# Performance work log

Measured on AMD Instinct MI355X. Metric: run time of the kernel, lower is better.

## Reference

```python
import jax, jax.numpy as jnp
import numpy as np

V = 780        # junction-tree vocab size
N = 50000      # total nodes in batch
M = 100001     # total messages (+1 null slot at index 0)
K = 6          # padded max neighbors
H = 256        # hidden size
B = 64         # number of trees (scope entries)
DEPTH = 6      # GRU depth


def setup_inputs() -> dict:
    key = jax.random.key(0)
    ks = jax.random.split(key, 12)
    p = lambda k, s: jax.random.normal(k, s, jnp.float32) * 0.02
    return {
        "fnode": jax.random.randint(ks[0], (N,), 0, V),
        "fmess": jax.random.randint(ks[1], (M,), 0, N),
        "node_graph": jax.random.randint(ks[2], (N, K), 0, M),
        "mess_graph": jax.random.randint(ks[3], (M, K), 0, M),
        "scope_st": jax.random.randint(ks[4], (B,), 0, N),
        "emb": p(ks[5], (V, H)),
        "Wz": p(ks[6], (H, 2 * H)), "bz": jnp.zeros((H,), jnp.float32),
        "Wr": p(ks[7], (H, H)),
        "Ur": p(ks[8], (H, H)), "bu": jnp.zeros((H,), jnp.float32),
        "Wh": p(ks[9], (H, 2 * H)), "bh": jnp.zeros((H,), jnp.float32),
        "Wo": p(ks[10], (H, 2 * H)), "bo": jnp.zeros((H,), jnp.float32),
    }


def reference(fnode, fmess, node_graph, mess_graph, scope_st,
              emb, Wz, bz, Wr, Ur, bu, Wh, bh, Wo, bo):
    fnode_e = emb[fnode]                       # [N, H] embedded node features
    x = fnode_e[fmess]                         # [M, H] per-message source features
    mask = jnp.ones((M, 1), jnp.float32).at[0].set(0.0)  # zero the null message
    # W_r(x) depends only on x; hoist it out of the loop (same math as original)
    xWr = (x @ Wr.T)[:, None, :]               # [M, 1, H]

    h = jnp.zeros((M, H), jnp.float32)
    for _ in range(DEPTH):
        h_nei = h[mess_graph]                  # [M, K, H] gather neighbor messages
        sum_h = h_nei.sum(axis=1)              # [M, H]
        z = jax.nn.sigmoid(jnp.concatenate([x, sum_h], axis=1) @ Wz.T + bz)
        r = jax.nn.sigmoid(xWr + h_nei @ Ur.T + bu)   # [M, K, H]
        sum_gated_h = (r * h_nei).sum(axis=1)  # [M, H]
        pre_h = jnp.tanh(jnp.concatenate([x, sum_gated_h], axis=1) @ Wh.T + bh)
        h = ((1.0 - z) * sum_h + z * pre_h) * mask

    mess_nei = h[node_graph].sum(axis=1)       # [N, H]
    node_vecs = jax.nn.relu(
        jnp.concatenate([fnode_e, mess_nei], axis=-1) @ Wo.T + bo)  # [N, H]
    tree_vecs = node_vecs[scope_st]            # [B, H] root vector per tree
    return tree_vecs, h
```

## Files before the change

kernel.cpp:

```cpp
#include <hip/hip_runtime.h>

typedef unsigned short u16;
typedef unsigned int   u32;
typedef short bf16x8 __attribute__((ext_vector_type(8)));
typedef float f32x4  __attribute__((ext_vector_type(4)));

#define V_ 780
#define N_ 50000
#define M_ 100001
#define K_ 6
#define H_ 256
#define B_ 64
#define DEPTH_ 6

typedef __attribute__((address_space(3))) u32 lds_u32;
typedef __attribute__((address_space(1))) const u32 glb_u32;
__device__ __forceinline__ void dma16(const void* g, void* l){
  __builtin_amdgcn_global_load_lds((glb_u32*)g, (lds_u32*)l, 16, 0, 0);
}

__device__ __forceinline__ float b2f(u16 u){
  union { u32 i; float f; } x; x.i = ((u32)u) << 16; return x.f;
}
__device__ __forceinline__ u16 f2b(float f){
  union { float f; u32 i; } x; x.f = f;
  u32 r = x.i + 0x7fffu + ((x.i >> 16) & 1u);
  return (u16)(r >> 16);
}
__device__ __forceinline__ float rcp_(float x){ return __builtin_amdgcn_rcpf(x); }
__device__ __forceinline__ float sigm(float x){ return rcp_(1.f + __expf(-x)); }
__device__ __forceinline__ float tanh_(float x){
  x = fminf(fmaxf(x, -15.f), 15.f);
  float e = __expf(2.f*x);
  return (e - 1.f) * rcp_(e + 1.f);
}
__device__ __forceinline__ int swz(int r){ return (r + (r >> 2)) & 3; }

__global__ void k_tables(const float* __restrict__ emb,
    const float* __restrict__ Wz, const float* __restrict__ bz,
    const float* __restrict__ Wr, const float* __restrict__ bu,
    const float* __restrict__ Wh, const float* __restrict__ bh,
    const float* __restrict__ Wo, const float* __restrict__ bo,
    float* __restrict__ tWz, float* __restrict__ tXr,
    float* __restrict__ tWh, float* __restrict__ tWo){
  int v = blockIdx.x, q = blockIdx.y, j = threadIdx.x;
  __shared__ float e[H_];
  e[j] = emb[v*H_ + j];
  __syncthreads();
  const float* w; const float* b; float* o; int ld;
  if      (q == 0){ w = Wz; b = bz; o = tWz; ld = 2*H_; }
  else if (q == 1){ w = Wr; b = bu; o = tXr; ld = H_;   }
  else if (q == 2){ w = Wh; b = bh; o = tWh; ld = 2*H_; }
  else            { w = Wo; b = bo; o = tWo; ld = 2*H_; }
  const float* wr = w + (size_t)j*ld;
  float a0 = 0.f, a1 = 0.f;
  #pragma unroll 4
  for (int i = 0; i < H_; i += 8){
    float4 x = *(const float4*)(wr + i);
    float4 y = *(const float4*)(wr + i + 4);
    a0 += e[i  ]*x.x + e[i+1]*x.y + e[i+2]*x.z + e[i+3]*x.w;
    a1 += e[i+4]*y.x + e[i+5]*y.y + e[i+6]*y.z + e[i+7]*y.w;
  }
  float val = a0 + a1 + b[j];
  if (q == 1) val = __expf(-val);
  o[v*H_ + j] = val;
}

__global__ void k_convw(const float* __restrict__ Ur, const float* __restrict__ Wz,
                        const float* __restrict__ Wh,
                        u16* __restrict__ Urb, u16* __restrict__ Wzb, u16* __restrict__ Whb){
  int r = blockIdx.x, j = threadIdx.x;
  Urb[r*H_ + j] = f2b(Ur[r*H_ + j]);
  Wzb[r*H_ + j] = f2b(Wz[r*(2*H_) + H_ + j]);
  Whb[r*H_ + j] = f2b(Wh[r*(2*H_) + H_ + j]);
}

__global__ void k_init(const int* __restrict__ fnode, const int* __restrict__ fmess,
                       const float* __restrict__ tWz, const float* __restrict__ tWh,
                       int* __restrict__ vmsg, u16* __restrict__ hb){
  int m = blockIdx.x, j = threadIdx.x;
  int v = fnode[fmess[m]];
  if (j == 0) vmsg[m] = v;
  float val = (m == 0) ? 0.f : sigm(tWz[v*H_ + j])*tanh_(tWh[v*H_ + j]);
  hb[(size_t)m*H_ + j] = f2b(val);
}

__global__ void k_gather(const u16* __restrict__ hb, const u16* __restrict__ Eb,
                         const int* __restrict__ mg, const int* __restrict__ vmsg,
                         const float* __restrict__ tXr,
                         u16* __restrict__ sumh, u16* __restrict__ sumg){
  int m = blockIdx.x*2 + (threadIdx.x >> 7);
  if (m >= M_) return;
  int tj = (threadIdx.x & 127) * 2;
  int v = vmsg[m];
  float2 X = *(const float2*)(tXr + (size_t)v*H_ + tj);
  const int2* mgp = (const int2*)(mg + m*K_);
  int2 g01 = mgp[0], g23 = mgp[1], g45 = mgp[2];
  int gs[K_] = {g01.x, g01.y, g23.x, g23.y, g45.x, g45.y};
  const char* hc = (const char*)hb;
  const char* ec = (const char*)Eb;
  const u32 cj = (u32)tj * 2u;
  float s0=0.f, s1=0.f, a0=0.f, a1=0.f;
  #pragma unroll
  for (int k=0;k<K_;k++){
    u32 off = ((u32)gs[k] << 9) + cj;
    u32 hp = *(const u32*)(hc + off);
    u32 ep = *(const u32*)(ec + off);
    float h0 = b2f((u16)hp), h1 = b2f((u16)(hp>>16));
    float e0 = b2f((u16)ep), e1 = b2f((u16)(ep>>16));
    s0 += h0; s1 += h1;
    a0 += rcp_(fmaf(X.x, e0, 1.f)) * h0;
    a1 += rcp_(fmaf(X.y, e1, 1.f)) * h1;
  }
  *(u32*)(sumh + (size_t)m*H_ + tj) = (u32)f2b(s0) | ((u32)f2b(s1)<<16);
  *(u32*)(sumg + (size_t)m*H_ + tj) = (u32)f2b(a0) | ((u32)f2b(a1)<<16);
}

__global__ __launch_bounds__(256,3) void k_gemm(
    const u16* __restrict__ A, const u16* __restrict__ W, u16* __restrict__ C){
  __shared__ __align__(16) u16 lA[2][64*32];
  __shared__ __align__(16) u16 lB[2][256*32];
  const int t    = threadIdx.x;
  const int m0   = blockIdx.x * 64;
  const int lane = t & 63, wave = t >> 6;
  const int l16  = lane & 15, kc8 = lane >> 4;

  const int rA = t >> 2, cA = t & 3;
  const int kA = (cA ^ swz(rA)) * 8;
  const int gmA = (m0 + rA < M_) ? (m0 + rA) : (M_ - 1);
  const int aOff = (wave*64)*8;
  int rB[4], kB[4], bOff[4];
  #pragma unroll
  for (int p=0;p<4;p++){
    int s = t + 256*p;
    rB[p] = s >> 2; int cc = s & 3;
    kB[p] = (cc ^ swz(rB[p])) * 8;
    bOff[p] = (wave*64 + 256*p)*8;
  }

  f32x4 acc[4][4];
  #pragma unroll
  for (int r=0;r<4;r++)
    #pragma unroll
    for (int c=0;c<4;c++)
      #pragma unroll
      for (int q=0;q<4;q++) acc[r][c][q] = 0.f;

  auto stage = [&](int buf, int k0){
    dma16(A + (size_t)gmA*H_ + k0 + kA, &lA[buf][aOff]);
    #pragma unroll
    for (int p=0;p<4;p++)
      dma16(W + (size_t)rB[p]*H_ + k0 + kB[p], &lB[buf][bOff[p]]);
  };

  stage(0, 0);
  __syncthreads();
  int cur = 0;
  for (int ks = 0; ks < 8; ++ks){
    if (ks < 7) stage(cur^1, (ks+1)*32);
    bf16x8 aF[4], bF[4];
    #pragma unroll
    for (int r=0;r<4;r++){
      int row = r*16 + l16;
      aF[r] = *(const bf16x8*)(&lA[cur][row*32 + ((kc8 ^ swz(row))*8)]);
    }
    #pragma unroll
    for (int c=0;c<4;c++){
      int row = wave*64 + c*16 + l16;
      bF[c] = *(const bf16x8*)(&lB[cur][row*32 + ((kc8 ^ swz(row))*8)]);
    }
    #pragma unroll
    for (int r=0;r<4;r++)
      #pragma unroll
      for (int c=0;c<4;c++)
        acc[r][c] = __builtin_amdgcn_mfma_f32_16x16x32_bf16(aF[r], bF[c], acc[r][c], 0,0,0);
    if (ks < 7) __syncthreads();
    cur ^= 1;
  }

  #pragma unroll
  for (int r=0;r<4;r++){
    #pragma unroll
    for (int c=0;c<4;c++){
      int mb = m0 + r*16 + kc8*4;
      int n  = wave*64 + c*16 + l16;
      #pragma unroll
      for (int q=0;q<4;q++){
        int m = mb + q;
        if (m < M_) C[(size_t)m*H_ + n] = f2b(__expf(-acc[r][c][q]));
      }
    }
  }
}

template<bool F32OUT>
__global__ __launch_bounds__(256,3) void k_gemmzh(
    const u16* __restrict__ sumh, const u16* __restrict__ sumg,
    const u16* __restrict__ Wzb, const u16* __restrict__ Whb,
    void* __restrict__ Cv,
    const float* __restrict__ tWz, const float* __restrict__ tWh,
    const int* __restrict__ vmsg){
  __shared__ __align__(16) u16 lH[2][64*32];
  __shared__ __align__(16) u16 lG[2][64*32];
  __shared__ __align__(16) u16 lZ[2][128*32];
  __shared__ __align__(16) u16 lW[2][128*32];
  const int t    = threadIdx.x;
  const int m0   = (blockIdx.x >> 1) * 64;
  const int n0   = (blockIdx.x & 1) * 128;
  const int lane = t & 63, wave = t >> 6;
  const int wrow = wave >> 1, wcol = wave & 1;
  const int l16  = lane & 15, kc8 = lane >> 4;

  const int rA = t >> 2, cA = t & 3;
  const int kA = (cA ^ swz(rA)) * 8;
  const int gmA = (m0 + rA < M_) ? (m0 + rA) : (M_ - 1);
  const int aOff = (wave*64)*8;
  int rB[2], kB[2], bOff[2];
  #pragma unroll
  for (int p=0;p<2;p++){
    int s = t + 256*p;
    rB[p] = s >> 2; int cc = s & 3;
    kB[p] = (cc ^ swz(rB[p])) * 8;
    bOff[p] = (wave*64 + 256*p)*8;
  }

  f32x4 accZ[2][4], accH[2][4];
  #pragma unroll
  for (int r=0;r<2;r++)
    #pragma unroll
    for (int c=0;c<4;c++)
      #pragma unroll
      for (int q=0;q<4;q++){ accZ[r][c][q] = 0.f; accH[r][c][q] = 0.f; }

  auto stage = [&](int buf, int k0){
    dma16(sumh + (size_t)gmA*H_ + k0 + kA, &lH[buf][aOff]);
    dma16(sumg + (size_t)gmA*H_ + k0 + kA, &lG[buf][aOff]);
    #pragma unroll
    for (int p=0;p<2;p++){
      dma16(Wzb + (size_t)(n0+rB[p])*H_ + k0 + kB[p], &lZ[buf][bOff[p]]);
      dma16(Whb + (size_t)(n0+rB[p])*H_ + k0 + kB[p], &lW[buf][bOff[p]]);
    }
  };

  stage(0, 0);
  __syncthreads();
  int cur = 0;
  for (int ks = 0; ks < 8; ++ks){
    if (ks < 7) stage(cur^1, (ks+1)*32);
    bf16x8 aH[2], aG[2];
    #pragma unroll
    for (int r=0;r<2;r++){
      int row = wrow*32 + r*16 + l16;
      int off = row*32 + ((kc8 ^ swz(row))*8);
      aH[r] = *(const bf16x8*)(&lH[cur][off]);
      aG[r] = *(const bf16x8*)(&lG[cur][off]);
    }
    #pragma unroll
    for (int c=0;c<4;c++){
      int row = wcol*64 + c*16 + l16;
      int off = row*32 + ((kc8 ^ swz(row))*8);
      bf16x8 bZ = *(const bf16x8*)(&lZ[cur][off]);
      bf16x8 bW = *(const bf16x8*)(&lW[cur][off]);
      #pragma unroll
      for (int r=0;r<2;r++){
        accZ[r][c] = __builtin_amdgcn_mfma_f32_16x16x32_bf16(aH[r], bZ, accZ[r][c], 0,0,0);
        accH[r][c] = __builtin_amdgcn_mfma_f32_16x16x32_bf16(aG[r], bW, accH[r][c], 0,0,0);
      }
    }
    if (ks < 7) __syncthreads();
    cur ^= 1;
  }

  #pragma unroll
  for (int r=0;r<2;r++){
    #pragma unroll
    for (int q=0;q<4;q++){
      int m = m0 + wrow*32 + r*16 + kc8*4 + q;
      if (m >= M_) continue;
      int v = vmsg[m];
      #pragma unroll
      for (int c=0;c<4;c++){
        int n = n0 + wcol*64 + c*16 + l16;
        float z   = sigm(tWz[v*H_ + n] + accZ[r][c][q]);
        float pre = tanh_(tWh[v*H_ + n] + accH[r][c][q]);
        float sh  = b2f(sumh[(size_t)m*H_ + n]);
        float o   = (m == 0) ? 0.f : (1.f - z)*sh + z*pre;
        if (F32OUT) ((float*)Cv)[(size_t)m*H_ + n] = o;
        else        ((u16*)Cv)[(size_t)m*H_ + n] = f2b(o);
      }
    }
  }
}

__global__ void k_final(const float* __restrict__ h, const int* __restrict__ ng,
                        const int* __restrict__ fnode, const int* __restrict__ scope,
                        const float* __restrict__ tWo, const float* __restrict__ Wo,
                        float* __restrict__ out){
  int b = blockIdx.x, j = threadIdx.x;
  int n = scope[b];
  __shared__ float mn[H_];
  float s = 0.f;
  #pragma unroll
  for (int k=0;k<K_;k++){
    int g = ng[n*K_ + k];
    s += h[(size_t)g*H_ + j];
  }
  mn[j] = s;
  __syncthreads();
  int v = fnode[n];
  float acc = tWo[v*H_ + j];
  const float* w = Wo + j*(2*H_) + H_;
  for (int i=0;i<H_;i+=4){
    float4 a = *(const float4*)(w+i);
    acc += mn[i]*a.x + mn[i+1]*a.y + mn[i+2]*a.z + mn[i+3]*a.w;
  }
  out[b*H_ + j] = fmaxf(acc, 0.f);
}

__global__ void k_zero(float* __restrict__ out, int n){
  int i = blockIdx.x*256 + threadIdx.x;
  int stride = gridDim.x*256;
  for (; i < n; i += stride) out[i] = 0.f;
}

extern "C" void kernel_launch(void* const* d_in, const int* in_sizes, int n_in,
                              void* d_out, int out_size, void* d_ws, size_t ws_size,
                              hipStream_t stream){
  const int* fnode      = (const int*)d_in[0];
  const int* fmess      = (const int*)d_in[1];
  const int* node_graph = (const int*)d_in[2];
  const int* mess_graph = (const int*)d_in[3];
  const int* scope_st   = (const int*)d_in[4];
  const float* emb = (const float*)d_in[5];
  const float* Wz  = (const float*)d_in[6];
  const float* bz  = (const float*)d_in[7];
  const float* Wr  = (const float*)d_in[8];
  const float* Ur  = (const float*)d_in[9];
  const float* bu  = (const float*)d_in[10];
  const float* Wh  = (const float*)d_in[11];
  const float* bh  = (const float*)d_in[12];
  const float* Wo  = (const float*)d_in[13];
  const float* bo  = (const float*)d_in[14];

  char* ws = (char*)d_ws;
  size_t off = 0;
  float* tWz = (float*)(ws + off); off += (size_t)V_*H_*4;
  float* tXr = (float*)(ws + off); off += (size_t)V_*H_*4;
  float* tWh = (float*)(ws + off); off += (size_t)V_*H_*4;
  float* tWo = (float*)(ws + off); off += (size_t)V_*H_*4;
  u16* Urb  = (u16*)(ws + off); off += (size_t)H_*H_*2;
  u16* Wzb  = (u16*)(ws + off); off += (size_t)H_*H_*2;
  u16* Whb  = (u16*)(ws + off); off += (size_t)H_*H_*2;
  int* vmsg = (int*)(ws + off); off += ((size_t)M_*4 + 511) & ~(size_t)511;
  u16* Eb   = (u16*)(ws + off); off += (size_t)M_*H_*2;
  u16* sumh = (u16*)(ws + off); off += (size_t)M_*H_*2;
  u16* sumg = (u16*)(ws + off); off += (size_t)M_*H_*2;

  if (ws_size < off){
    k_zero<<<2048, 256, 0, stream>>>((float*)d_out, out_size);
    return;
  }

  float* out = (float*)d_out;
  float* h   = out + (size_t)B_*H_;
  u16*   hb  = (u16*)h;

  const int MT64 = (M_ + 63)/64;
  const int GG   = 2*MT64;

  k_tables<<<dim3(V_,4), H_, 0, stream>>>(emb, Wz, bz, Wr, bu, Wh, bh, Wo, bo,
                                          tWz, tXr, tWh, tWo);
  k_convw<<<H_, H_, 0, stream>>>(Ur, Wz, Wh, Urb, Wzb, Whb);
  k_init<<<M_, H_, 0, stream>>>(fnode, fmess, tWz, tWh, vmsg, hb);

  for (int it = 0; it < DEPTH_-1; ++it){
    k_gemm<<<MT64, 256, 0, stream>>>(hb, Urb, Eb);
    k_gather<<<(M_+1)/2, 256, 0, stream>>>(hb, Eb, mess_graph, vmsg, tXr, sumh, sumg);
    if (it < DEPTH_-2)
      k_gemmzh<false><<<GG, 256, 0, stream>>>(sumh, sumg, Wzb, Whb, hb,
                                              tWz, tWh, vmsg);
    else
      k_gemmzh<true ><<<GG, 256, 0, stream>>>(sumh, sumg, Wzb, Whb, h,
                                              tWz, tWh, vmsg);
  }

  k_final<<<B_, H_, 0, stream>>>(h, node_graph, fnode, scope_st, tWo, Wo, out);
}
```

Before: 1.364 ms.

## Interleave h and Ur-gate rows in one buffer for contiguous neighbor gathers

Stores each message's bf16 hidden state and its exp(-h·Ur) values side by side in a single row of 512 elements inside the output buffer, and drops the separate E workspace. The gather kernel now reads one contiguous 1 KB span per neighbor instead of two separate 512 B rows. It also maps one wave per message, with each lane doing 8-byte loads and stores. The GEMM now reads and writes disjoint column halves of the same buffer, so its __restrict__ qualifiers are removed. The aim is better DRAM and cache-line locality in the random-access gather, at the cost of a doubled row stride for the GEMM's A loads and stores.

```diff
diff --git a/kernel.cpp b/kernel.cpp
--- a/kernel.cpp
+++ b/kernel.cpp
@@ -12,6 +12,8 @@
 #define H_ 256
 #define B_ 64
 #define DEPTH_ 6
+
+#define HE_LD 512
 
 typedef __attribute__((address_space(3))) u32 lds_u32;
 typedef __attribute__((address_space(1))) const u32 glb_u32;
@@ -77,47 +79,55 @@
 
 __global__ void k_init(const int* __restrict__ fnode, const int* __restrict__ fmess,
                        const float* __restrict__ tWz, const float* __restrict__ tWh,
-                       int* __restrict__ vmsg, u16* __restrict__ hb){
+                       int* __restrict__ vmsg, u16* __restrict__ hE){
   int m = blockIdx.x, j = threadIdx.x;
   int v = fnode[fmess[m]];
   if (j == 0) vmsg[m] = v;
   float val = (m == 0) ? 0.f : sigm(tWz[v*H_ + j])*tanh_(tWh[v*H_ + j]);
-  hb[(size_t)m*H_ + j] = f2b(val);
-}
-
-__global__ void k_gather(const u16* __restrict__ hb, const u16* __restrict__ Eb,
+  hE[(size_t)m*HE_LD + j] = f2b(val);
+}
+
+__global__ void k_gather(const u16* __restrict__ hE,
                          const int* __restrict__ mg, const int* __restrict__ vmsg,
                          const float* __restrict__ tXr,
                          u16* __restrict__ sumh, u16* __restrict__ sumg){
-  int m = blockIdx.x*2 + (threadIdx.x >> 7);
+  int m = blockIdx.x*4 + (threadIdx.x >> 6);
   if (m >= M_) return;
-  int tj = (threadIdx.x & 127) * 2;
+  const int lane = threadIdx.x & 63;
   int v = vmsg[m];
-  float2 X = *(const float2*)(tXr + (size_t)v*H_ + tj);
+  float4 X = *(const float4*)(tXr + (size_t)v*H_ + lane*4);
   const int2* mgp = (const int2*)(mg + m*K_);
   int2 g01 = mgp[0], g23 = mgp[1], g45 = mgp[2];
   int gs[K_] = {g01.x, g01.y, g23.x, g23.y, g45.x, g45.y};
-  const char* hc = (const char*)hb;
-  const char* ec = (const char*)Eb;
-  const u32 cj = (u32)tj * 2u;
-  float s0=0.f, s1=0.f, a0=0.f, a1=0.f;
+  const char* bc = (const char*)hE;
+  const u32 cb = (u32)lane * 8u;
+  float s0=0.f,s1=0.f,s2=0.f,s3=0.f, a0=0.f,a1=0.f,a2=0.f,a3=0.f;
   #pragma unroll
   for (int k=0;k<K_;k++){
-    u32 off = ((u32)gs[k] << 9) + cj;
-    u32 hp = *(const u32*)(hc + off);
-    u32 ep = *(const u32*)(ec + off);
-    float h0 = b2f((u16)hp), h1 = b2f((u16)(hp>>16));
-    float e0 = b2f((u16)ep), e1 = b2f((u16)(ep>>16));
-    s0 += h0; s1 += h1;
-    a0 += rcp_(fmaf(X.x, e0, 1.f)) * h0;
-    a1 += rcp_(fmaf(X.y, e1, 1.f)) * h1;
-  }
-  *(u32*)(sumh + (size_t)m*H_ + tj) = (u32)f2b(s0) | ((u32)f2b(s1)<<16);
-  *(u32*)(sumg + (size_t)m*H_ + tj) = (u32)f2b(a0) | ((u32)f2b(a1)<<16);
+    u32 off = ((u32)gs[k] << 10) + cb;
+    uint2 hp = *(const uint2*)(bc + off);
+    uint2 ep = *(const uint2*)(bc + off + 512);
+    float h0=b2f((u16)hp.x), h1=b2f((u16)(hp.x>>16));
+    float h2=b2f((u16)hp.y), h3=b2f((u16)(hp.y>>16));
+    float e0=b2f((u16)ep.x), e1=b2f((u16)(ep.x>>16));
+    float e2=b2f((u16)ep.y), e3=b2f((u16)(ep.y>>16));
+    s0+=h0; s1+=h1; s2+=h2; s3+=h3;
+    a0 += rcp_(fmaf(X.x,e0,1.f))*h0;
+    a1 += rcp_(fmaf(X.y,e1,1.f))*h1;
+    a2 += rcp_(fmaf(X.z,e2,1.f))*h2;
+    a3 += rcp_(fmaf(X.w,e3,1.f))*h3;
+  }
+  uint2 sh, sg;
+  sh.x = (u32)f2b(s0) | ((u32)f2b(s1)<<16);
+  sh.y = (u32)f2b(s2) | ((u32)f2b(s3)<<16);
+  sg.x = (u32)f2b(a0) | ((u32)f2b(a1)<<16);
+  sg.y = (u32)f2b(a2) | ((u32)f2b(a3)<<16);
+  *(uint2*)((char*)sumh + ((size_t)m<<9) + cb) = sh;
+  *(uint2*)((char*)sumg + ((size_t)m<<9) + cb) = sg;
 }
 
 __global__ __launch_bounds__(256,3) void k_gemm(
-    const u16* __restrict__ A, const u16* __restrict__ W, u16* __restrict__ C){
+    const u16* A, const u16* __restrict__ W, u16* C){
   __shared__ __align__(16) u16 lA[2][64*32];
   __shared__ __align__(16) u16 lB[2][256*32];
   const int t    = threadIdx.x;
@@ -147,7 +157,7 @@
       for (int q=0;q<4;q++) acc[r][c][q] = 0.f;
 
   auto stage = [&](int buf, int k0){
-    dma16(A + (size_t)gmA*H_ + k0 + kA, &lA[buf][aOff]);
+    dma16(A + (size_t)gmA*HE_LD + k0 + kA, &lA[buf][aOff]);
     #pragma unroll
     for (int p=0;p<4;p++)
       dma16(W + (size_t)rB[p]*H_ + k0 + kB[p], &lB[buf][bOff[p]]);
@@ -187,7 +197,7 @@
       #pragma unroll
       for (int q=0;q<4;q++){
         int m = mb + q;
-        if (m < M_) C[(size_t)m*H_ + n] = f2b(__expf(-acc[r][c][q]));
+        if (m < M_) C[(size_t)m*HE_LD + H_ + n] = f2b(__expf(-acc[r][c][q]));
       }
     }
   }
@@ -286,7 +296,7 @@
         float sh  = b2f(sumh[(size_t)m*H_ + n]);
         float o   = (m == 0) ? 0.f : (1.f - z)*sh + z*pre;
         if (F32OUT) ((float*)Cv)[(size_t)m*H_ + n] = o;
-        else        ((u16*)Cv)[(size_t)m*H_ + n] = f2b(o);
+        else        ((u16*)Cv)[(size_t)m*HE_LD + n] = f2b(o);
       }
     }
   }
@@ -352,7 +362,6 @@
   u16* Wzb  = (u16*)(ws + off); off += (size_t)H_*H_*2;
   u16* Whb  = (u16*)(ws + off); off += (size_t)H_*H_*2;
   int* vmsg = (int*)(ws + off); off += ((size_t)M_*4 + 511) & ~(size_t)511;
-  u16* Eb   = (u16*)(ws + off); off += (size_t)M_*H_*2;
   u16* sumh = (u16*)(ws + off); off += (size_t)M_*H_*2;
   u16* sumg = (u16*)(ws + off); off += (size_t)M_*H_*2;
 
@@ -363,7 +372,7 @@
 
   float* out = (float*)d_out;
   float* h   = out + (size_t)B_*H_;
-  u16*   hb  = (u16*)h;
+  u16* hE = (u16*)h;
 
   const int MT64 = (M_ + 63)/64;
   const int GG   = 2*MT64;
@@ -371,13 +380,13 @@
   k_tables<<<dim3(V_,4), H_, 0, stream>>>(emb, Wz, bz, Wr, bu, Wh, bh, Wo, bo,
                                           tWz, tXr, tWh, tWo);
   k_convw<<<H_, H_, 0, stream>>>(Ur, Wz, Wh, Urb, Wzb, Whb);
-  k_init<<<M_, H_, 0, stream>>>(fnode, fmess, tWz, tWh, vmsg, hb);
+  k_init<<<M_, H_, 0, stream>>>(fnode, fmess, tWz, tWh, vmsg, hE);
 
   for (int it = 0; it < DEPTH_-1; ++it){
-    k_gemm<<<MT64, 256, 0, stream>>>(hb, Urb, Eb);
-    k_gather<<<(M_+1)/2, 256, 0, stream>>>(hb, Eb, mess_graph, vmsg, tXr, sumh, sumg);
+    k_gemm<<<MT64, 256, 0, stream>>>(hE, Urb, hE);
+    k_gather<<<(M_+3)/4, 256, 0, stream>>>(hE, mess_graph, vmsg, tXr, sumh, sumg);
     if (it < DEPTH_-2)
-      k_gemmzh<false><<<GG, 256, 0, stream>>>(sumh, sumg, Wzb, Whb, hb,
+      k_gemmzh<false><<<GG, 256, 0, stream>>>(sumh, sumg, Wzb, Whb, hE,
                                               tWz, tWh, vmsg);
     else
       k_gemmzh<true ><<<GG, 256, 0, stream>>>(sumh, sumg, Wzb, Whb, h,
```

Result: no change. 1.361 ms (-0.2%).
